# Optimization experiments

Hardware: AMD Instinct MI355X
Metric: run time of the kernel (lower is better)

The kernel has to match this reference:

```python
import jax, jax.numpy as jnp
import numpy as np

N_USERS = 20000
N_ENT = 80000
N_NODES = N_USERS + N_ENT
D = 64
N_REL_ROWS = 2 * 16 + 1  # 2*n_relations + 1
E = 1_250_000
N_LAYERS = 2
EPS_ATT = 1e-9
EPS_NORM = 1e-12


def setup_inputs() -> dict:
    key = jax.random.key(0)
    k = jax.random.split(key, 8)
    return {
        "user_emb": jax.random.normal(k[0], (N_USERS, D), jnp.float32) * 0.1,
        "entity_emb": jax.random.normal(k[1], (N_ENT, D), jnp.float32) * 0.1,
        "rel_emb": jax.random.normal(k[2], (N_REL_ROWS, D), jnp.float32) * 0.1,
        "W1": jax.random.normal(k[3], (D, D), jnp.float32) * (1.0 / np.sqrt(D)),
        "W2": jax.random.normal(k[4], (D, D), jnp.float32) * (1.0 / np.sqrt(D)),
        "src": jax.random.randint(k[5], (E,), 0, N_NODES, jnp.int32),
        "dst": jax.random.randint(k[6], (E,), 0, N_NODES, jnp.int32),
        "rel": jax.random.randint(k[7], (E,), 0, N_REL_ROWS, jnp.int32),
    }


def reference(user_emb, entity_emb, rel_emb, W1, W2, src, dst, rel):
    n_users = user_emb.shape[0]
    n_nodes = n_users + entity_emb.shape[0]
    lrelu = lambda x: jax.nn.leaky_relu(x, 0.01)

    ego = jnp.concatenate([user_emb, entity_emb], axis=0)  # [N, D]
    embs = [ego]
    r_e = rel_emb[rel]  # [E, D] constant across layers
    for _ in range(N_LAYERS):
        h = ego[src]  # [E, D]
        t = ego[dst]  # [E, D]
        # attention logits + per-src-node segment softmax
        logits = lrelu(jnp.sum(h * t * r_e, axis=1))  # [E]
        mx = jax.ops.segment_max(logits, src, num_segments=n_nodes)  # [N]
        ex = jnp.exp(logits - mx[src])
        denom = jax.ops.segment_sum(ex, src, num_segments=n_nodes)
        att = ex / (denom[src] + EPS_ATT)
        # message + scatter-add aggregation (mess_dropout=0 / eval mode)
        msg = t * att[:, None]  # [E, D]
        aggr = jax.ops.segment_sum(msg, src, num_segments=n_nodes)  # [N, D]
        # bi-interaction aggregator
        new = lrelu((ego + aggr) @ W1 + (ego * aggr) @ W2)
        new = new / jnp.maximum(
            jnp.linalg.norm(new, axis=1, keepdims=True), EPS_NORM)
        embs.append(new)
        ego = new
    final = jnp.mean(jnp.stack(embs, axis=1), axis=1)  # [N, D]
    item_res = final[n_users:]
    user_res = final[:n_users]
    return item_res, user_res
```

## Files before the change

kernel.cpp:

```cpp
#include <hip/hip_runtime.h>
#include <hip/hip_bf16.h>
#include <math.h>

#define N_USERS 20000
#define N_ENT   80000
#define N_NODES 100000
#define D 64
#define N_REL 33
#define E_EDGES 1250000
#define ELLW 40
#define EPS_ATT 1e-9f
#define EPS_NORM 1e-12f
#define RELP 68
#define LW 8
#define NPB (LW*2)
#define N_XCD 8
#define NODES_PER_XCD (N_NODES / N_XCD)

__device__ __forceinline__ int out_row(int n){
  return (n >= N_USERS) ? (n - N_USERS) : (n + N_ENT);
}
__device__ __forceinline__ unsigned short f2bf(float f){
  unsigned u = __float_as_uint(f);
  return (unsigned short)((u + 0x7FFFu + ((u >> 16) & 1u)) >> 16);
}
__device__ __forceinline__ float bf2f(unsigned short b){
  return __uint_as_float(((unsigned)b) << 16);
}
__device__ __forceinline__ float4 bfq(uint2 u){
  float4 r;
  r.x = __uint_as_float(u.x << 16);
  r.y = __uint_as_float(u.x & 0xFFFF0000u);
  r.z = __uint_as_float(u.y << 16);
  r.w = __uint_as_float(u.y & 0xFFFF0000u);
  return r;
}

__global__ void k_zero(unsigned* __restrict__ cnt){
  int i = blockIdx.x*blockDim.x + threadIdx.x;
  if (i < N_NODES) cnt[i] = 0u;
}

__global__ void k_init_scatter(const float* __restrict__ user, const float* __restrict__ ent,
                               const float* __restrict__ W1, const float* __restrict__ W2,
                               const int* __restrict__ src, const int* __restrict__ dst,
                               const int* __restrict__ rel,
                               unsigned short* __restrict__ ego, unsigned* __restrict__ wpack,
                               unsigned* __restrict__ cnt, unsigned* __restrict__ spack){
  int stride = gridDim.x*blockDim.x;
  int tid0 = blockIdx.x*blockDim.x + threadIdx.x;
  for (int i = tid0; i < D*D/2; i += stride){
    int e0 = i*2;
    int c = e0 >> 8, j = (e0 >> 2) & 63, e = e0 & 3;
    int s0 = (4*c+e)*64 + j, s1 = (4*c+e+1)*64 + j;
    wpack[i]         = (unsigned)f2bf(W1[s0]) | ((unsigned)f2bf(W1[s1]) << 16);
    wpack[D*D/2 + i] = (unsigned)f2bf(W2[s0]) | ((unsigned)f2bf(W2[s1]) << 16);
  }
  const int total4 = N_NODES * D / 4;
  for (int i = tid0; i < total4; i += stride){
    int idx = i*4, n = idx >> 6, d = idx & 63;
    float4 v = (n < N_USERS) ? *(const float4*)(user + (size_t)n*D + d)
                             : *(const float4*)(ent + (size_t)(n-N_USERS)*D + d);
    uint2 p;
    p.x = (unsigned)f2bf(v.x) | ((unsigned)f2bf(v.y) << 16);
    p.y = (unsigned)f2bf(v.z) | ((unsigned)f2bf(v.w) << 16);
    *(uint2*)(ego + idx) = p;
  }
  int xcd = blockIdx.x & (N_XCD-1);
  int rank = blockIdx.x >> 3;
  int nlo = xcd * NODES_PER_XCD, nhi = nlo + NODES_PER_XCD;
  const int e4 = E_EDGES / 4;
  int et = rank*256 + threadIdx.x;
  int estride = (gridDim.x >> 3) * 256;
  for (int i = et; i < e4; i += estride){
    int4 s = ((const int4*)src)[i];
    int4 d = ((const int4*)dst)[i];
    int4 r = ((const int4*)rel)[i];
    unsigned p;
    if (s.x >= nlo && s.x < nhi){
      p = atomicAdd(&cnt[s.x], 1u);
      if (p < ELLW) spack[(size_t)s.x*ELLW + p] = ((unsigned)r.x << 17) | (unsigned)d.x;
    }
    if (s.y >= nlo && s.y < nhi){
      p = atomicAdd(&cnt[s.y], 1u);
      if (p < ELLW) spack[(size_t)s.y*ELLW + p] = ((unsigned)r.y << 17) | (unsigned)d.y;
    }
    if (s.z >= nlo && s.z < nhi){
      p = atomicAdd(&cnt[s.z], 1u);
      if (p < ELLW) spack[(size_t)s.z*ELLW + p] = ((unsigned)r.z << 17) | (unsigned)d.z;
    }
    if (s.w >= nlo && s.w < nhi){
      p = atomicAdd(&cnt[s.w], 1u);
      if (p < ELLW) spack[(size_t)s.w*ELLW + p] = ((unsigned)r.w << 17) | (unsigned)d.w;
    }
  }
}

template<bool FINAL>
__global__ __launch_bounds__(512, 7) void k_layer(const unsigned* __restrict__ cnt,
    const unsigned* __restrict__ spack, const unsigned* __restrict__ wpack,
    const float* __restrict__ relE,
    const unsigned short* __restrict__ egoin, unsigned short* __restrict__ egoout,
    const unsigned short* __restrict__ ego0, float* __restrict__ out){
  __shared__ unsigned sW1b[D*D/2], sW2b[D*D/2];
  __shared__ float srel[N_REL*RELP];
  __shared__ float sx1[NPB][D], sx2[NPB][D];
  int tid = threadIdx.x;
  for (int i = tid; i < D*D/2; i += 512){
    sW1b[i] = wpack[i];
    sW2b[i] = wpack[D*D/2 + i];
  }
  for (int i = tid; i < N_REL*D; i += 512){
    int r = i >> 6, k = i & 63;
    srel[r*RELP + k] = relE[i];
  }
  __syncthreads();

  int wave = tid >> 6, lane = tid & 63;
  int g = lane >> 4, q4 = (lane & 15) * 4;
  int slotA = wave*2, slotB = slotA + 1;
  int nA = blockIdx.x*NPB + slotA, nB = nA + 1;

  unsigned lenA = cnt[nA]; lenA = lenA < ELLW ? lenA : ELLW;
  unsigned lenB = cnt[nB]; lenB = lenB < ELLW ? lenB : ELLW;
  unsigned slotsA = (lenA + 3u) & ~3u;
  unsigned slotsB = (lenB + 3u) & ~3u;
  unsigned total  = slotsA + slotsB;
  unsigned baseA = (unsigned)nA * ELLW, baseB = (unsigned)nB * ELLW;

  float4 hA = bfq(*(const uint2*)(egoin + (size_t)nA*D + q4));
  float4 hB = bfq(*(const uint2*)(egoin + (size_t)nB*D + q4));

  float dn = 0.f;
  float4 ac = make_float4(0.f,0.f,0.f,0.f);
  float4 aA = make_float4(0.f,0.f,0.f,0.f);
  float4 aB = make_float4(0.f,0.f,0.f,0.f);
  bool flA = false;

  auto flush = [&](float4& aOut){
    #pragma unroll
    for (int m = 16; m <= 32; m <<= 1){
      dn   += __shfl_xor(dn,   m, 64);
      ac.x += __shfl_xor(ac.x, m, 64); ac.y += __shfl_xor(ac.y, m, 64);
      ac.z += __shfl_xor(ac.z, m, 64); ac.w += __shfl_xor(ac.w, m, 64);
    }
    float inv = 1.f / (dn + EPS_ATT);
    aOut = make_float4(ac.x*inv, ac.y*inv, ac.z*inv, ac.w*inv);
    dn = 0.f; ac = make_float4(0.f,0.f,0.f,0.f);
  };

  for (unsigned cb = 0; cb < total; cb += 64u){
    unsigned s = cb + (unsigned)lane;
    bool pA = s < slotsA;
    int ia = (int)s;            ia = ia < (int)lenA - 1 ? ia : (int)lenA - 1;
    int ib = (int)(s - slotsA); ib = ib < (int)lenB - 1 ? ib : (int)lenB - 1;
    ia = ia > 0 ? ia : 0;
    ib = ib > 0 ? ib : 0;
    unsigned pidx = pA ? (baseA + (unsigned)ia) : (baseB + (unsigned)ib);
    unsigned pk_pre = spack[pidx];

    unsigned rem = total - cb;
    unsigned cmax = rem < 64u ? rem : 64u;
    unsigned aRem = slotsA > cb ? slotsA - cb : 0u;
    int nitA = (int)((aRem < cmax ? aRem : cmax) >> 2);
    int nitT = (int)(cmax >> 2);

    #pragma unroll 1
    for (int ph = 0; ph < 2; ++ph){
      int it0 = ph ? nitA : 0;
      int it1 = ph ? nitT : nitA;
      float4 h = ph ? hB : hA;
      unsigned len = ph ? lenB : lenA;
      unsigned sBase = ph ? slotsA : 0u;
      for (int it = it0; it < it1; ++it){
        int sl = (it << 2) + g;
        unsigned pk = (unsigned)__builtin_amdgcn_ds_bpermute(sl << 2, (int)pk_pre);
        unsigned eidx = cb + (unsigned)sl - sBase;
        uint2 u = *(const uint2*)(egoin + (size_t)(pk & 0x1FFFFu)*D + q4);
        float4 rv = *(const float4*)&srel[(pk >> 17)*RELP + q4];
        float4 t = bfq(u);
        float p = (h.x*t.x)*rv.x;
        p = fmaf(h.y*t.y, rv.y, p);
        p = fmaf(h.z*t.z, rv.z, p);
        p = fmaf(h.w*t.w, rv.w, p);
        #pragma unroll
        for (int m = 1; m <= 8; m <<= 1) p += __shfl_xor(p, m, 64);
        float l = fmaxf(p, 0.01f*p);
        float ex = (eidx < len) ? __expf(l) : 0.f;
        dn += ex;
        ac.x = fmaf(ex, t.x, ac.x); ac.y = fmaf(ex, t.y, ac.y);
        ac.z = fmaf(ex, t.z, ac.z); ac.w = fmaf(ex, t.w, ac.w);
      }
      if (ph == 0 && !flA && slotsA <= cb + cmax){ flush(aA); flA = true; }
    }
  }
  if (!flA) flush(aA);
  flush(aB);

  if (g == 0){
    *(float4*)&sx1[slotA][q4] = make_float4(hA.x+aA.x, hA.y+aA.y, hA.z+aA.z, hA.w+aA.w);
    *(float4*)&sx2[slotA][q4] = make_float4(hA.x*aA.x, hA.y*aA.y, hA.z*aA.z, hA.w*aA.w);
    *(float4*)&sx1[slotB][q4] = make_float4(hB.x+aB.x, hB.y+aB.y, hB.z+aB.z, hB.w+aB.w);
    *(float4*)&sx2[slotB][q4] = make_float4(hB.x*aB.x, hB.y*aB.y, hB.z*aB.z, hB.w*aB.w);
  }

  float nvA = 0.f, nvB = 0.f;
  #pragma unroll
  for (int c = 0; c < 16; ++c){
    float4 w1 = bfq(*(const uint2*)&sW1b[c*128 + lane*2]);
    float4 w2 = bfq(*(const uint2*)&sW2b[c*128 + lane*2]);
    float4 xa1 = *(const float4*)&sx1[slotA][c*4];
    float4 xa2 = *(const float4*)&sx2[slotA][c*4];
    float4 xb1 = *(const float4*)&sx1[slotB][c*4];
    float4 xb2 = *(const float4*)&sx2[slotB][c*4];
    nvA = fmaf(xa1.x, w1.x, nvA); nvA = fmaf(xa1.y, w1.y, nvA);
    nvA = fmaf(xa1.z, w1.z, nvA); nvA = fmaf(xa1.w, w1.w, nvA);
    nvA = fmaf(xa2.x, w2.x, nvA); nvA = fmaf(xa2.y, w2.y, nvA);
    nvA = fmaf(xa2.z, w2.z, nvA); nvA = fmaf(xa2.w, w2.w, nvA);
    nvB = fmaf(xb1.x, w1.x, nvB); nvB = fmaf(xb1.y, w1.y, nvB);
    nvB = fmaf(xb1.z, w1.z, nvB); nvB = fmaf(xb1.w, w1.w, nvB);
    nvB = fmaf(xb2.x, w2.x, nvB); nvB = fmaf(xb2.y, w2.y, nvB);
    nvB = fmaf(xb2.z, w2.z, nvB); nvB = fmaf(xb2.w, w2.w, nvB);
  }
  nvA = fmaxf(nvA, 0.01f*nvA);
  nvB = fmaxf(nvB, 0.01f*nvB);
  float s2A = nvA*nvA, s2B = nvB*nvB;
  #pragma unroll
  for (int m = 1; m <= 32; m <<= 1){
    s2A += __shfl_xor(s2A, m, 64);
    s2B += __shfl_xor(s2B, m, 64);
  }
  nvA = nvA / fmaxf(sqrtf(s2A), EPS_NORM);
  nvB = nvB / fmaxf(sqrtf(s2B), EPS_NORM);

  if (FINAL){
    float z0A = bf2f(ego0[(size_t)nA*D + lane]);
    float z1A = bf2f(egoin[(size_t)nA*D + lane]);
    float z0B = bf2f(ego0[(size_t)nB*D + lane]);
    float z1B = bf2f(egoin[(size_t)nB*D + lane]);
    out[(size_t)out_row(nA)*D + lane] = (z0A + z1A + nvA) * (1.f/3.f);
    out[(size_t)out_row(nB)*D + lane] = (z0B + z1B + nvB) * (1.f/3.f);
  } else {
    egoout[(size_t)nA*D + lane] = f2bf(nvA);
    egoout[(size_t)nB*D + lane] = f2bf(nvB);
  }
}

extern "C" void kernel_launch(void* const* d_in, const int* in_sizes, int n_in,
                              void* d_out, int out_size, void* d_ws, size_t ws_size,
                              hipStream_t stream) {
  const float* user = (const float*)d_in[0];
  const float* ent  = (const float*)d_in[1];
  const float* relE = (const float*)d_in[2];
  const float* W1   = (const float*)d_in[3];
  const float* W2   = (const float*)d_in[4];
  const int*   src  = (const int*)d_in[5];
  const int*   dst  = (const int*)d_in[6];
  const int*   rel  = (const int*)d_in[7];
  float* out = (float*)d_out;

  char* ws = (char*)d_ws;
  unsigned short* ego0 = (unsigned short*)ws; ws += (size_t)N_NODES*D*sizeof(unsigned short);
  unsigned short* ego1 = (unsigned short*)ws; ws += (size_t)N_NODES*D*sizeof(unsigned short);
  unsigned* spack = (unsigned*)ws;            ws += (size_t)N_NODES*ELLW*sizeof(unsigned);
  unsigned* cnt = (unsigned*)ws;              ws += (size_t)N_NODES*sizeof(unsigned);
  unsigned* wpack = (unsigned*)ws;            ws += (size_t)D*D*sizeof(unsigned);

  k_zero<<<(N_NODES+255)/256, 256, 0, stream>>>(cnt);
  k_init_scatter<<<2048, 256, 0, stream>>>(user, ent, W1, W2, src, dst, rel,
                                           ego0, wpack, cnt, spack);

  const int lb = N_NODES / NPB;
  k_layer<false><<<lb, 512, 0, stream>>>(cnt, spack, wpack, relE, ego0, ego1, ego0, out);
  k_layer<true ><<<lb, 512, 0, stream>>>(cnt, spack, wpack, relE, ego1, ego1, ego0, out);
}
```

Before: 355.5 us.

## Use bf16 MFMA for bi-interaction transform with 32 nodes per block

Each block now handles 32 nodes, with each wave aggregating 4 nodes one at a time instead of interleaving two per wave. The aggregated [x+a, x*a] rows are stored as bf16 in shared memory. The dense W1/W2 transform then runs as a 16x16x32 bf16 MFMA over K=128, and a cross-wave shared-memory reduction produces the row norms. This removes the scalar FMA matvec and the per-block LDS staging of the weights, which are now read pre-swizzled from global memory. In exchange it rounds the MFMA inputs to bf16, adds block-wide barriers, and loses the packing of two nodes' edges into one 64-lane chunk.

```diff
diff --git a/kernel.cpp b/kernel.cpp
--- a/kernel.cpp
+++ b/kernel.cpp
@@ -12,10 +12,13 @@
 #define EPS_ATT 1e-9f
 #define EPS_NORM 1e-12f
 #define RELP 68
-#define LW 8
-#define NPB (LW*2)
+#define NPB 32
+#define SXP 136
 #define N_XCD 8
 #define NODES_PER_XCD (N_NODES / N_XCD)
+
+typedef __attribute__((ext_vector_type(8))) short bf16x8;
+typedef __attribute__((ext_vector_type(4))) float f32x4;
 
 __device__ __forceinline__ int out_row(int n){
   return (n >= N_USERS) ? (n - N_USERS) : (n + N_ENT);
@@ -45,16 +48,17 @@
                                const float* __restrict__ W1, const float* __restrict__ W2,
                                const int* __restrict__ src, const int* __restrict__ dst,
                                const int* __restrict__ rel,
-                               unsigned short* __restrict__ ego, unsigned* __restrict__ wpack,
+                               unsigned short* __restrict__ ego, unsigned short* __restrict__ wfrag,
                                unsigned* __restrict__ cnt, unsigned* __restrict__ spack){
   int stride = gridDim.x*blockDim.x;
   int tid0 = blockIdx.x*blockDim.x + threadIdx.x;
-  for (int i = tid0; i < D*D/2; i += stride){
-    int e0 = i*2;
-    int c = e0 >> 8, j = (e0 >> 2) & 63, e = e0 & 3;
-    int s0 = (4*c+e)*64 + j, s1 = (4*c+e+1)*64 + j;
-    wpack[i]         = (unsigned)f2bf(W1[s0]) | ((unsigned)f2bf(W1[s1]) << 16);
-    wpack[D*D/2 + i] = (unsigned)f2bf(W2[s0]) | ((unsigned)f2bf(W2[s1]) << 16);
+  for (int i = tid0; i < 8192; i += stride){
+    int ii = i & 7, l = (i >> 3) & 63, st = i >> 9;
+    int s = st >> 2, t = st & 3;
+    int k = 32*s + 8*(l >> 4) + ii;
+    int nn = 16*t + (l & 15);
+    float wv = (k < 64) ? W1[k*64 + nn] : W2[(k-64)*64 + nn];
+    wfrag[i] = f2bf(wv);
   }
   const int total4 = N_NODES * D / 4;
   for (int i = tid0; i < total4; i += stride){
@@ -98,18 +102,14 @@
 
 template<bool FINAL>
 __global__ __launch_bounds__(512, 7) void k_layer(const unsigned* __restrict__ cnt,
-    const unsigned* __restrict__ spack, const unsigned* __restrict__ wpack,
+    const unsigned* __restrict__ spack, const unsigned short* __restrict__ wfrag,
     const float* __restrict__ relE,
     const unsigned short* __restrict__ egoin, unsigned short* __restrict__ egoout,
     const unsigned short* __restrict__ ego0, float* __restrict__ out){
-  __shared__ unsigned sW1b[D*D/2], sW2b[D*D/2];
   __shared__ float srel[N_REL*RELP];
-  __shared__ float sx1[NPB][D], sx2[NPB][D];
+  __shared__ unsigned short sX[NPB][SXP];
+  __shared__ float part[2][16][4];
   int tid = threadIdx.x;
-  for (int i = tid; i < D*D/2; i += 512){
-    sW1b[i] = wpack[i];
-    sW2b[i] = wpack[D*D/2 + i];
-  }
   for (int i = tid; i < N_REL*D; i += 512){
     int r = i >> 6, k = i & 63;
     srel[r*RELP + k] = relE[i];
@@ -118,26 +118,37 @@
 
   int wave = tid >> 6, lane = tid & 63;
   int g = lane >> 4, q4 = (lane & 15) * 4;
-  int slotA = wave*2, slotB = slotA + 1;
-  int nA = blockIdx.x*NPB + slotA, nB = nA + 1;
-
-  unsigned lenA = cnt[nA]; lenA = lenA < ELLW ? lenA : ELLW;
-  unsigned lenB = cnt[nB]; lenB = lenB < ELLW ? lenB : ELLW;
-  unsigned slotsA = (lenA + 3u) & ~3u;
-  unsigned slotsB = (lenB + 3u) & ~3u;
-  unsigned total  = slotsA + slotsB;
-  unsigned baseA = (unsigned)nA * ELLW, baseB = (unsigned)nB * ELLW;
-
-  float4 hA = bfq(*(const uint2*)(egoin + (size_t)nA*D + q4));
-  float4 hB = bfq(*(const uint2*)(egoin + (size_t)nB*D + q4));
-
-  float dn = 0.f;
-  float4 ac = make_float4(0.f,0.f,0.f,0.f);
-  float4 aA = make_float4(0.f,0.f,0.f,0.f);
-  float4 aB = make_float4(0.f,0.f,0.f,0.f);
-  bool flA = false;
-
-  auto flush = [&](float4& aOut){
+  int n0 = blockIdx.x*NPB + wave*4;
+
+  for (int v = 0; v < 4; ++v){
+    int n = n0 + v;
+    unsigned len = cnt[n]; len = len < ELLW ? len : ELLW;
+    int pli = (int)len - 1;
+    int li = lane < pli ? lane : pli;
+    li = li > 0 ? li : 0;
+    unsigned pk_pre = spack[(size_t)n*ELLW + li];
+    float4 h = bfq(*(const uint2*)(egoin + (size_t)n*D + q4));
+    float dn = 0.f;
+    float4 ac = make_float4(0.f,0.f,0.f,0.f);
+    int nit = (int)((len + 3u) >> 2);
+    for (int it = 0; it < nit; ++it){
+      int sl = (it << 2) + g;
+      unsigned pk = (unsigned)__builtin_amdgcn_ds_bpermute(sl << 2, (int)pk_pre);
+      uint2 u = *(const uint2*)(egoin + (size_t)(pk & 0x1FFFFu)*D + q4);
+      float4 rv = *(const float4*)&srel[(pk >> 17)*RELP + q4];
+      float4 t = bfq(u);
+      float p = (h.x*t.x)*rv.x;
+      p = fmaf(h.y*t.y, rv.y, p);
+      p = fmaf(h.z*t.z, rv.z, p);
+      p = fmaf(h.w*t.w, rv.w, p);
+      #pragma unroll
+      for (int m = 1; m <= 8; m <<= 1) p += __shfl_xor(p, m, 64);
+      float l = fmaxf(p, 0.01f*p);
+      float ex = (sl < (int)len) ? __expf(l) : 0.f;
+      dn += ex;
+      ac.x = fmaf(ex, t.x, ac.x); ac.y = fmaf(ex, t.y, ac.y);
+      ac.z = fmaf(ex, t.z, ac.z); ac.w = fmaf(ex, t.w, ac.w);
+    }
     #pragma unroll
     for (int m = 16; m <= 32; m <<= 1){
       dn   += __shfl_xor(dn,   m, 64);
@@ -145,104 +156,64 @@
       ac.z += __shfl_xor(ac.z, m, 64); ac.w += __shfl_xor(ac.w, m, 64);
     }
     float inv = 1.f / (dn + EPS_ATT);
-    aOut = make_float4(ac.x*inv, ac.y*inv, ac.z*inv, ac.w*inv);
-    dn = 0.f; ac = make_float4(0.f,0.f,0.f,0.f);
-  };
-
-  for (unsigned cb = 0; cb < total; cb += 64u){
-    unsigned s = cb + (unsigned)lane;
-    bool pA = s < slotsA;
-    int ia = (int)s;            ia = ia < (int)lenA - 1 ? ia : (int)lenA - 1;
-    int ib = (int)(s - slotsA); ib = ib < (int)lenB - 1 ? ib : (int)lenB - 1;
-    ia = ia > 0 ? ia : 0;
-    ib = ib > 0 ? ib : 0;
-    unsigned pidx = pA ? (baseA + (unsigned)ia) : (baseB + (unsigned)ib);
-    unsigned pk_pre = spack[pidx];
-
-    unsigned rem = total - cb;
-    unsigned cmax = rem < 64u ? rem : 64u;
-    unsigned aRem = slotsA > cb ? slotsA - cb : 0u;
-    int nitA = (int)((aRem < cmax ? aRem : cmax) >> 2);
-    int nitT = (int)(cmax >> 2);
-
-    #pragma unroll 1
-    for (int ph = 0; ph < 2; ++ph){
-      int it0 = ph ? nitA : 0;
-      int it1 = ph ? nitT : nitA;
-      float4 h = ph ? hB : hA;
-      unsigned len = ph ? lenB : lenA;
-      unsigned sBase = ph ? slotsA : 0u;
-      for (int it = it0; it < it1; ++it){
-        int sl = (it << 2) + g;
-        unsigned pk = (unsigned)__builtin_amdgcn_ds_bpermute(sl << 2, (int)pk_pre);
-        unsigned eidx = cb + (unsigned)sl - sBase;
-        uint2 u = *(const uint2*)(egoin + (size_t)(pk & 0x1FFFFu)*D + q4);
-        float4 rv = *(const float4*)&srel[(pk >> 17)*RELP + q4];
-        float4 t = bfq(u);
-        float p = (h.x*t.x)*rv.x;
-        p = fmaf(h.y*t.y, rv.y, p);
-        p = fmaf(h.z*t.z, rv.z, p);
-        p = fmaf(h.w*t.w, rv.w, p);
-        #pragma unroll
-        for (int m = 1; m <= 8; m <<= 1) p += __shfl_xor(p, m, 64);
-        float l = fmaxf(p, 0.01f*p);
-        float ex = (eidx < len) ? __expf(l) : 0.f;
-        dn += ex;
-        ac.x = fmaf(ex, t.x, ac.x); ac.y = fmaf(ex, t.y, ac.y);
-        ac.z = fmaf(ex, t.z, ac.z); ac.w = fmaf(ex, t.w, ac.w);
-      }
-      if (ph == 0 && !flA && slotsA <= cb + cmax){ flush(aA); flA = true; }
-    }
-  }
-  if (!flA) flush(aA);
-  flush(aB);
-
-  if (g == 0){
-    *(float4*)&sx1[slotA][q4] = make_float4(hA.x+aA.x, hA.y+aA.y, hA.z+aA.z, hA.w+aA.w);
-    *(float4*)&sx2[slotA][q4] = make_float4(hA.x*aA.x, hA.y*aA.y, hA.z*aA.z, hA.w*aA.w);
-    *(float4*)&sx1[slotB][q4] = make_float4(hB.x+aB.x, hB.y+aB.y, hB.z+aB.z, hB.w+aB.w);
-    *(float4*)&sx2[slotB][q4] = make_float4(hB.x*aB.x, hB.y*aB.y, hB.z*aB.z, hB.w*aB.w);
-  }
-
-  float nvA = 0.f, nvB = 0.f;
-  #pragma unroll
-  for (int c = 0; c < 16; ++c){
-    float4 w1 = bfq(*(const uint2*)&sW1b[c*128 + lane*2]);
-    float4 w2 = bfq(*(const uint2*)&sW2b[c*128 + lane*2]);
-    float4 xa1 = *(const float4*)&sx1[slotA][c*4];
-    float4 xa2 = *(const float4*)&sx2[slotA][c*4];
-    float4 xb1 = *(const float4*)&sx1[slotB][c*4];
-    float4 xb2 = *(const float4*)&sx2[slotB][c*4];
-    nvA = fmaf(xa1.x, w1.x, nvA); nvA = fmaf(xa1.y, w1.y, nvA);
-    nvA = fmaf(xa1.z, w1.z, nvA); nvA = fmaf(xa1.w, w1.w, nvA);
-    nvA = fmaf(xa2.x, w2.x, nvA); nvA = fmaf(xa2.y, w2.y, nvA);
-    nvA = fmaf(xa2.z, w2.z, nvA); nvA = fmaf(xa2.w, w2.w, nvA);
-    nvB = fmaf(xb1.x, w1.x, nvB); nvB = fmaf(xb1.y, w1.y, nvB);
-    nvB = fmaf(xb1.z, w1.z, nvB); nvB = fmaf(xb1.w, w1.w, nvB);
-    nvB = fmaf(xb2.x, w2.x, nvB); nvB = fmaf(xb2.y, w2.y, nvB);
-    nvB = fmaf(xb2.z, w2.z, nvB); nvB = fmaf(xb2.w, w2.w, nvB);
-  }
-  nvA = fmaxf(nvA, 0.01f*nvA);
-  nvB = fmaxf(nvB, 0.01f*nvB);
-  float s2A = nvA*nvA, s2B = nvB*nvB;
-  #pragma unroll
-  for (int m = 1; m <= 32; m <<= 1){
-    s2A += __shfl_xor(s2A, m, 64);
-    s2B += __shfl_xor(s2B, m, 64);
-  }
-  nvA = nvA / fmaxf(sqrtf(s2A), EPS_NORM);
-  nvB = nvB / fmaxf(sqrtf(s2B), EPS_NORM);
-
-  if (FINAL){
-    float z0A = bf2f(ego0[(size_t)nA*D + lane]);
-    float z1A = bf2f(egoin[(size_t)nA*D + lane]);
-    float z0B = bf2f(ego0[(size_t)nB*D + lane]);
-    float z1B = bf2f(egoin[(size_t)nB*D + lane]);
-    out[(size_t)out_row(nA)*D + lane] = (z0A + z1A + nvA) * (1.f/3.f);
-    out[(size_t)out_row(nB)*D + lane] = (z0B + z1B + nvB) * (1.f/3.f);
-  } else {
-    egoout[(size_t)nA*D + lane] = f2bf(nvA);
-    egoout[(size_t)nB*D + lane] = f2bf(nvB);
+    if (g == 0){
+      float4 a = make_float4(ac.x*inv, ac.y*inv, ac.z*inv, ac.w*inv);
+      int nloc = wave*4 + v;
+      unsigned p0 = (unsigned)f2bf(h.x + a.x) | ((unsigned)f2bf(h.y + a.y) << 16);
+      unsigned p1 = (unsigned)f2bf(h.z + a.z) | ((unsigned)f2bf(h.w + a.w) << 16);
+      unsigned p2 = (unsigned)f2bf(h.x * a.x) | ((unsigned)f2bf(h.y * a.y) << 16);
+      unsigned p3 = (unsigned)f2bf(h.z * a.z) | ((unsigned)f2bf(h.w * a.w) << 16);
+      *(unsigned*)&sX[nloc][q4]          = p0;
+      *(unsigned*)&sX[nloc][q4 + 2]      = p1;
+      *(unsigned*)&sX[nloc][64 + q4]     = p2;
+      *(unsigned*)&sX[nloc][64 + q4 + 2] = p3;
+    }
+  }
+  __syncthreads();
+
+  int mt = wave >> 2, nt = wave & 3;
+  f32x4 acc = {0.f, 0.f, 0.f, 0.f};
+  int arow = mt*16 + (lane & 15);
+  int kg = (lane >> 4) * 8;
+  #pragma unroll
+  for (int s = 0; s < 4; ++s){
+    bf16x8 af = *(const bf16x8*)&sX[arow][s*32 + kg];
+    bf16x8 bfg = *(const bf16x8*)&wfrag[(size_t)(((s << 2) | nt)*64 + lane)*8];
+    acc = __builtin_amdgcn_mfma_f32_16x16x32_bf16(af, bfg, acc, 0, 0, 0);
+  }
+  float y[4], ss[4];
+  #pragma unroll
+  for (int r = 0; r < 4; ++r){
+    float t = acc[r];
+    t = fmaxf(t, 0.01f*t);
+    y[r] = t; ss[r] = t*t;
+  }
+  #pragma unroll
+  for (int m = 1; m <= 8; m <<= 1){
+    #pragma unroll
+    for (int r = 0; r < 4; ++r) ss[r] += __shfl_xor(ss[r], m, 64);
+  }
+  if ((lane & 15) == 0){
+    int rbase = (lane >> 4) * 4;
+    #pragma unroll
+    for (int r = 0; r < 4; ++r) part[mt][rbase + r][nt] = ss[r];
+  }
+  __syncthreads();
+  int col = nt*16 + (lane & 15);
+  #pragma unroll
+  for (int r = 0; r < 4; ++r){
+    int rrow = (lane >> 4)*4 + r;
+    float4 ps = *(const float4*)&part[mt][rrow][0];
+    float nrm = sqrtf(ps.x + ps.y + ps.z + ps.w);
+    float yv = y[r] / fmaxf(nrm, EPS_NORM);
+    int n = blockIdx.x*NPB + mt*16 + rrow;
+    if (FINAL){
+      float z0 = bf2f(ego0[(size_t)n*D + col]);
+      float z1 = bf2f(egoin[(size_t)n*D + col]);
+      out[(size_t)out_row(n)*D + col] = (z0 + z1 + yv) * (1.f/3.f);
+    } else {
+      egoout[(size_t)n*D + col] = f2bf(yv);
+    }
   }
 }
 
@@ -260,17 +231,17 @@
   float* out = (float*)d_out;
 
   char* ws = (char*)d_ws;
-  unsigned short* ego0 = (unsigned short*)ws; ws += (size_t)N_NODES*D*sizeof(unsigned short);
-  unsigned short* ego1 = (unsigned short*)ws; ws += (size_t)N_NODES*D*sizeof(unsigned short);
-  unsigned* spack = (unsigned*)ws;            ws += (size_t)N_NODES*ELLW*sizeof(unsigned);
-  unsigned* cnt = (unsigned*)ws;              ws += (size_t)N_NODES*sizeof(unsigned);
-  unsigned* wpack = (unsigned*)ws;            ws += (size_t)D*D*sizeof(unsigned);
+  unsigned short* ego0 = (unsigned short*)ws;  ws += (size_t)N_NODES*D*sizeof(unsigned short);
+  unsigned short* ego1 = (unsigned short*)ws;  ws += (size_t)N_NODES*D*sizeof(unsigned short);
+  unsigned* spack = (unsigned*)ws;             ws += (size_t)N_NODES*ELLW*sizeof(unsigned);
+  unsigned* cnt = (unsigned*)ws;               ws += (size_t)N_NODES*sizeof(unsigned);
+  unsigned short* wfrag = (unsigned short*)ws; ws += (size_t)8192*sizeof(unsigned short);
 
   k_zero<<<(N_NODES+255)/256, 256, 0, stream>>>(cnt);
   k_init_scatter<<<2048, 256, 0, stream>>>(user, ent, W1, W2, src, dst, rel,
-                                           ego0, wpack, cnt, spack);
+                                           ego0, wfrag, cnt, spack);
 
   const int lb = N_NODES / NPB;
-  k_layer<false><<<lb, 512, 0, stream>>>(cnt, spack, wpack, relE, ego0, ego1, ego0, out);
-  k_layer<true ><<<lb, 512, 0, stream>>>(cnt, spack, wpack, relE, ego1, ego1, ego0, out);
-}
+  k_layer<false><<<lb, 512, 0, stream>>>(cnt, spack, wfrag, relE, ego0, ego1, ego0, out);
+  k_layer<true ><<<lb, 512, 0, stream>>>(cnt, spack, wfrag, relE, ego1, ego1, ego0, out);
+}
```

New measurement: 284.5 us. -20.0%, faster.
